# Optimization experiments

Measured on AMD Instinct MI355X. Metric: run time of the kernel, lower is better.

## Reference

```python
import jax, jax.numpy as jnp
import numpy as np

D = 2048
N_HEADS = 16
N_KV = 4
HEAD_DIM = D // N_HEADS  # 128
N_REP = N_HEADS // N_KV  # 4
B, S = 2, 2048


def setup_inputs() -> dict:
    key = jax.random.key(0)
    ks = jax.random.split(key, 5)
    scale = 0.02
    return {
        "x": jax.random.normal(ks[0], (B, S, D), dtype=jnp.float32),
        "wq": jax.random.normal(ks[1], (D, N_HEADS * HEAD_DIM), dtype=jnp.float32) * scale,
        "wk": jax.random.normal(ks[2], (D, N_KV * HEAD_DIM), dtype=jnp.float32) * scale,
        "wv": jax.random.normal(ks[3], (D, N_KV * HEAD_DIM), dtype=jnp.float32) * scale,
        "wo": jax.random.normal(ks[4], (N_HEADS * HEAD_DIM, D), dtype=jnp.float32) * scale,
    }


def reference(x, wq, wk, wv, wo):
    b, s, _ = x.shape
    # projections
    xq = (x @ wq).reshape(b, s, N_HEADS, HEAD_DIM)
    xk = (x @ wk).reshape(b, s, N_KV, HEAD_DIM)
    xv = (x @ wv).reshape(b, s, N_KV, HEAD_DIM)
    # GQA: group queries per kv head -> [b, n_kv, n_rep, s, d]
    xq = xq.transpose(0, 2, 1, 3).reshape(b, N_KV, N_REP, s, HEAD_DIM)
    xk = xk.transpose(0, 2, 1, 3)  # [b, n_kv, s, d]
    xv = xv.transpose(0, 2, 1, 3)
    scale = 1.0 / jnp.sqrt(jnp.asarray(HEAD_DIM, dtype=x.dtype))
    scores = jnp.einsum('bkrqd,bkvd->bkrqv', xq, xk) * scale  # [b,n_kv,n_rep,s,s]
    causal = jnp.triu(jnp.ones((s, s), dtype=bool), k=1)
    scores = jnp.where(causal, jnp.asarray(-jnp.inf, dtype=scores.dtype), scores)
    probs = jax.nn.softmax(scores, axis=-1)
    out = jnp.einsum('bkrqv,bkvd->bkrqd', probs, xv)  # [b,n_kv,n_rep,s,d]
    out = out.reshape(b, N_HEADS, s, HEAD_DIM).transpose(0, 2, 1, 3).reshape(b, s, N_HEADS * HEAD_DIM)
    return out @ wo
```

## Files before the change

### kernel.cpp

```cpp
#include <hip/hip_runtime.h>

typedef unsigned short u16;
using bf16x8 = __attribute__((ext_vector_type(8))) short;
using f32x4  = __attribute__((ext_vector_type(4))) float;

#define ATTN_NEG (-3.0e38f)

__device__ __forceinline__ u16 f2bf_rne(float f) {
  unsigned int u = __float_as_uint(f);
  u += 0x7fffu + ((u >> 16) & 1u);
  return (u16)(u >> 16);
}

__device__ __forceinline__ void load_lds16(const u16* g, u16* l) {
  using gp = const __attribute__((address_space(1))) unsigned int*;
  using lp = __attribute__((address_space(3))) unsigned int*;
  __builtin_amdgcn_global_load_lds((gp)g, (lp)l, 16, 0, 0);
}

__device__ __forceinline__ void transpose_body(const float* __restrict__ in,
                                               u16* __restrict__ out, int K, int N,
                                               int bx, int by, int tid) {
  __shared__ float tile[32][33];
  int tx = tid & 31, ty = tid >> 5;
  int x0 = bx * 32, y0 = by * 32;
  #pragma unroll
  for (int i = 0; i < 32; i += 8)
    tile[ty + i][tx] = in[(size_t)(y0 + ty + i) * N + x0 + tx];
  __syncthreads();
  #pragma unroll
  for (int i = 0; i < 32; i += 8)
    out[(size_t)(x0 + ty + i) * K + y0 + tx] = f2bf_rne(tile[tx][ty + i]);
}

__global__ __launch_bounds__(256) void prep_kernel(const float* __restrict__ x,
                                                   const float* __restrict__ wq,
                                                   const float* __restrict__ wk,
                                                   const float* __restrict__ wv,
                                                   const float* __restrict__ wo,
                                                   u16* xb, u16* wqt, u16* wkt, u16* wvt,
                                                   u16* wot) {
  int bid = blockIdx.x, tid = threadIdx.x;
  if (bid < 8192) {
    int i = bid * 1024 + tid * 4;
    float4 v = *(const float4*)(x + i);
    u16* p = xb + i;
    p[0] = f2bf_rne(v.x); p[1] = f2bf_rne(v.y); p[2] = f2bf_rne(v.z); p[3] = f2bf_rne(v.w);
  } else if (bid < 12288) {
    int t = bid - 8192;
    transpose_body(wq, wqt, 2048, 2048, t & 63, t >> 6, tid);
  } else if (bid < 13312) {
    int t = bid - 12288;
    transpose_body(wk, wkt, 2048, 512, t & 15, t >> 4, tid);
  } else if (bid < 14336) {
    int t = bid - 13312;
    transpose_body(wv, wvt, 2048, 512, t & 15, t >> 4, tid);
  } else {
    int t = bid - 14336;
    transpose_body(wo, wot, 2048, 2048, t & 63, t >> 6, tid);
  }
}

template <int MODE>
__device__ __forceinline__ void gemm_tile(const u16* __restrict__ A, const u16* __restrict__ Bt,
                                          void* __restrict__ Cv, int M, int N, int K,
                                          int bx, int by, char* smem) {
  u16* As = (u16*)smem;
  u16* Bs = (u16*)(smem + 8192);
  const int tid  = threadIdx.x;
  const int wave = tid >> 6, lane = tid & 63;
  const int quad = lane >> 4, l16 = lane & 15;
  const int m0 = by * 128, n0 = bx * 128;
  const int wm = (wave >> 1) * 64, wn = (wave & 1) * 64;
  f32x4 acc[4][4] = {};

  const int srow = (wave << 4) + (lane >> 2);
  const int scol = (lane & 3) << 3;
  const u16* ga0 = A  + (size_t)(m0 + srow) * K + scol;
  const u16* gb0 = Bt + (size_t)(n0 + srow) * K + scol;
  u16* la = As + wave * 512;
  u16* lb = Bs + wave * 512;

  for (int k0 = 0; k0 < K; k0 += 32) {
    __syncthreads();
    load_lds16(ga0 + k0, la);
    load_lds16(ga0 + (size_t)64 * K + k0, la + 2048);
    load_lds16(gb0 + k0, lb);
    load_lds16(gb0 + (size_t)64 * K + k0, lb + 2048);
    __syncthreads();
    bf16x8 af[4], bfr[4];
    #pragma unroll
    for (int i = 0; i < 4; ++i) {
      af[i]  = *(const bf16x8*)(As + (wm + i * 16 + l16) * 32 + quad * 8);
      bfr[i] = *(const bf16x8*)(Bs + (wn + i * 16 + l16) * 32 + quad * 8);
    }
    #pragma unroll
    for (int mi = 0; mi < 4; ++mi)
      #pragma unroll
      for (int ni = 0; ni < 4; ++ni)
        acc[mi][ni] = __builtin_amdgcn_mfma_f32_16x16x32_bf16(af[mi], bfr[ni], acc[mi][ni], 0, 0, 0);
  }

  if constexpr (MODE == 0 || MODE == 3) {
    const float sc = (MODE == 3) ? 0.12751742f : 1.0f;
    u16* Cb = (u16*)Cv;
    #pragma unroll
    for (int mi = 0; mi < 4; ++mi)
      #pragma unroll
      for (int ni = 0; ni < 4; ++ni) {
        int row = m0 + wm + mi * 16 + quad * 4;
        int col = n0 + wn + ni * 16 + l16;
        #pragma unroll
        for (int r = 0; r < 4; ++r)
          Cb[(size_t)(row + r) * N + col] = f2bf_rne(acc[mi][ni][r] * sc);
      }
  } else if constexpr (MODE == 1) {
    u16* Cb = (u16*)Cv;
    #pragma unroll
    for (int mi = 0; mi < 4; ++mi)
      #pragma unroll
      for (int ni = 0; ni < 4; ++ni) {
        int col = n0 + wn + ni * 16 + l16;
        #pragma unroll
        for (int r = 0; r < 4; ++r) {
          int row = m0 + wm + mi * 16 + quad * 4 + r;
          int bb = row >> 11, s = row & 2047;
          Cb[((size_t)(bb * 512 + col)) * 2048 + s] = f2bf_rne(acc[mi][ni][r]);
        }
      }
  } else {
    float* Cf = (float*)Cv;
    #pragma unroll
    for (int mi = 0; mi < 4; ++mi)
      #pragma unroll
      for (int ni = 0; ni < 4; ++ni) {
        int row = m0 + wm + mi * 16 + quad * 4;
        int col = n0 + wn + ni * 16 + l16;
        #pragma unroll
        for (int r = 0; r < 4; ++r)
          Cf[(size_t)(row + r) * N + col] = acc[mi][ni][r];
      }
  }
}

__global__ __launch_bounds__(256) void qkv_gemm(const u16* xb, const u16* wqt, const u16* wkt,
                                                const u16* wvt, u16* Qb, u16* Kb, u16* Vt) {
  extern __shared__ char smem[];
  int bx = blockIdx.x, by = blockIdx.y;
  if (bx < 16)
    gemm_tile<3>(xb, wqt, Qb, 4096, 2048, 2048, bx, by, smem);
  else if (bx < 20)
    gemm_tile<0>(xb, wkt, Kb, 4096, 512, 2048, bx - 16, by, smem);
  else
    gemm_tile<1>(xb, wvt, Vt, 4096, 512, 2048, bx - 20, by, smem);
}

template <int MODE>
__global__ __launch_bounds__(256) void gemm_kernel(const u16* A, const u16* Bt, void* C,
                                                   int M, int N, int K) {
  extern __shared__ char smem[];
  gemm_tile<MODE>(A, Bt, C, M, N, K, blockIdx.x, blockIdx.y, smem);
}


__device__ __forceinline__ void stage_kv(const u16* __restrict__ Kg, const u16* __restrict__ Vg,
                                         int kt0, u16* __restrict__ kbuf, u16* __restrict__ vbuf,
                                         int wave, int quad, int l16) {
  if (wave == 0) {
    #pragma unroll
    for (int ks = 0; ks < 4; ++ks)
      #pragma unroll
      for (int h = 0; h < 2; ++h)
        load_lds16(Kg + (size_t)(kt0 + h * 16 + l16) * 512 + ks * 32 + quad * 8,
                   kbuf + (ks * 2 + h) * 512);
  } else {
    #pragma unroll
    for (int f = 0; f < 8; ++f)
      load_lds16(Vg + (size_t)(16 * f + l16) * 2048 + kt0 + quad * 8, vbuf + f * 512);
  }
}

template <bool MASKED>
__device__ __forceinline__ void attn_compute(const u16* __restrict__ kbuf,
                                             const u16* __restrict__ vbuf,
                                             u16* __restrict__ pw, int kt0, int q0w,
                                             int quad, int l16, const bf16x8 (&qf)[4],
                                             f32x4 (&o)[8], float (&l_part)[4]) {
  const bool have1 = !MASKED || ((q0w & 16) != 0);
  const int slot = (quad * 16 + l16) * 8;
  f32x4 sa0 = {}, sa1 = {};
  #pragma unroll
  for (int ks = 0; ks < 4; ++ks) {
    bf16x8 kf0 = *(const bf16x8*)(kbuf + (ks * 2) * 512 + slot);
    sa0 = __builtin_amdgcn_mfma_f32_16x16x32_bf16(qf[ks], kf0, sa0, 0, 0, 0);
  }
  if (have1) {
    #pragma unroll
    for (int ks = 0; ks < 4; ++ks) {
      bf16x8 kf1 = *(const bf16x8*)(kbuf + (ks * 2 + 1) * 512 + slot);
      sa1 = __builtin_amdgcn_mfma_f32_16x16x32_bf16(qf[ks], kf1, sa1, 0, 0, 0);
    }
  }

  float p0[4], p1[4];
  #pragma unroll
  for (int r = 0; r < 4; ++r) {
    float s0, s1;
    if (MASKED) {
      int qpos = q0w + quad * 4 + r;
      s0 = (kt0 + l16 <= qpos) ? sa0[r] : ATTN_NEG;
      s1 = (have1 && (kt0 + 16 + l16 <= qpos)) ? sa1[r] : ATTN_NEG;
    } else {
      s0 = sa0[r];
      s1 = sa1[r];
    }
    p0[r] = __builtin_amdgcn_exp2f(s0);
    p1[r] = __builtin_amdgcn_exp2f(s1);
    l_part[r] += p0[r] + p1[r];
  }
  #pragma unroll
  for (int r = 0; r < 4; ++r) {
    pw[(quad * 4 + r) * 40 + l16]      = f2bf_rne(p0[r]);
    pw[(quad * 4 + r) * 40 + 16 + l16] = f2bf_rne(p1[r]);
  }
  __builtin_amdgcn_wave_barrier();
  bf16x8 pf = *(const bf16x8*)(pw + l16 * 40 + quad * 8);
  #pragma unroll
  for (int f = 0; f < 8; ++f) {
    bf16x8 vf = *(const bf16x8*)(vbuf + f * 512 + slot);
    o[f] = __builtin_amdgcn_mfma_f32_16x16x32_bf16(pf, vf, o[f], 0, 0, 0);
  }
}

__global__ __launch_bounds__(128, 2) void attn_kernel(const u16* __restrict__ Qb,
                                                      const u16* __restrict__ Kb,
                                                      const u16* __restrict__ Vt,
                                                      u16* __restrict__ Ob) {
  constexpr int S = 2048;
  const int b = blockIdx.z, h = blockIdx.y, g = h >> 2, tp = blockIdx.x;
  const int tid = threadIdx.x;
  const int wave = tid >> 6, lane = tid & 63, quad = lane >> 4, l16 = lane & 15;
  __shared__ alignas(16) u16 Kt[2][4096];
  __shared__ alignas(16) u16 Vl[2][4096];
  __shared__ alignas(16) u16 Pl[2][640];

  const u16* Kg = Kb + (size_t)b * S * 512 + g * 128;
  const u16* Vg = Vt + (size_t)(b * 512 + g * 128) * 2048;
  u16* pw = &Pl[wave][0];

  #pragma unroll
  for (int half = 0; half < 2; ++half) {
    const int tile = (half == 0) ? tp : 63 - tp;
    const int q0w = tile * 32 + wave * 16;
    const int nsteps = tile + 1;

    bf16x8 qf[4];
    const u16* qrow = Qb + (size_t)(b * S + q0w + l16) * 2048 + h * 128 + quad * 8;
    #pragma unroll
    for (int ks = 0; ks < 4; ++ks) qf[ks] = *(const bf16x8*)(qrow + ks * 32);

    f32x4 o[8] = {};
    float l_part[4] = {0.f, 0.f, 0.f, 0.f};

    __syncthreads();
    stage_kv(Kg, Vg, 0, Kt[0], Vl[0], wave, quad, l16);

    for (int s = 0; s < nsteps; ++s) {
      __syncthreads();
      if (s + 1 < nsteps)
        stage_kv(Kg, Vg, (s + 1) * 32, Kt[(s + 1) & 1], Vl[(s + 1) & 1], wave, quad, l16);
      if (s < nsteps - 1)
        attn_compute<false>(Kt[s & 1], Vl[s & 1], pw, s * 32, q0w, quad, l16, qf, o, l_part);
      else
        attn_compute<true>(Kt[s & 1], Vl[s & 1], pw, s * 32, q0w, quad, l16, qf, o, l_part);
    }

    #pragma unroll
    for (int d = 1; d < 16; d <<= 1) {
      #pragma unroll
      for (int r = 0; r < 4; ++r) l_part[r] += __shfl_xor(l_part[r], d);
    }
    float il[4];
    #pragma unroll
    for (int r = 0; r < 4; ++r) il[r] = 1.f / l_part[r];
    u16* orow = Ob + (size_t)(b * S + q0w + quad * 4) * 2048 + h * 128 + l16;
    #pragma unroll
    for (int f = 0; f < 8; ++f)
      #pragma unroll
      for (int r = 0; r < 4; ++r)
        orow[(size_t)r * 2048 + f * 16] = f2bf_rne(o[f][r] * il[r]);
  }
}

extern "C" void kernel_launch(void* const* d_in, const int* in_sizes, int n_in,
                              void* d_out, int out_size, void* d_ws, size_t ws_size,
                              hipStream_t stream) {
  const float* x  = (const float*)d_in[0];
  const float* wq = (const float*)d_in[1];
  const float* wk = (const float*)d_in[2];
  const float* wv = (const float*)d_in[3];
  const float* wo = (const float*)d_in[4];
  float* out = (float*)d_out;
  char* ws = (char*)d_ws;

  u16* xb  = (u16*)(ws);
  u16* wqt = (u16*)(ws + 16777216);
  u16* wkt = (u16*)(ws + 25165824);
  u16* wvt = (u16*)(ws + 27262976);
  u16* wot = (u16*)(ws + 29360128);
  u16* Qb  = (u16*)(ws + 37748736);
  u16* Kb  = (u16*)(ws + 54525952);
  u16* Vt  = (u16*)(ws + 58720256);
  u16* Ab  = (u16*)(ws + 62914560);

  prep_kernel<<<18432, 256, 0, stream>>>(x, wq, wk, wv, wo, xb, wqt, wkt, wvt, wot);
  qkv_gemm<<<dim3(24, 32), 256, 16384, stream>>>(xb, wqt, wkt, wvt, Qb, Kb, Vt);
  attn_kernel<<<dim3(32, 16, 2), 128, 0, stream>>>(Qb, Kb, Vt, Ab);
  gemm_kernel<2><<<dim3(16, 32), 256, 16384, stream>>>(Ab, wot, out, 4096, 2048, 2048);
}
```

Measured before the change: 348.0 us.

## Enlarge attention query tile to 128 rows with 4 waves sharing K/V stages

The attention kernel now uses 256-thread blocks covering 128 query rows. Each wave handles two 16-row query subtiles against the same K fragments in registers, so each staged K/V tile is reused across four times as many queries. All four waves now share the K/V staging loads. Causal skipping is done per wave using a diagonal step index, and tile pairing (tp, 15-tp) keeps the load balanced. The trade-offs are fewer blocks (256 instead of 1024), higher register pressure at occupancy 1, and waves that sit idle past their diagonal step but still hit the barriers.

After: 341.1 us. 1.02x faster.

```diff
diff --git a/kernel.cpp b/kernel.cpp
--- a/kernel.cpp
+++ b/kernel.cpp
@@ -166,73 +166,78 @@
 __device__ __forceinline__ void stage_kv(const u16* __restrict__ Kg, const u16* __restrict__ Vg,
                                          int kt0, u16* __restrict__ kbuf, u16* __restrict__ vbuf,
                                          int wave, int quad, int l16) {
-  if (wave == 0) {
-    #pragma unroll
-    for (int ks = 0; ks < 4; ++ks)
-      #pragma unroll
-      for (int h = 0; h < 2; ++h)
-        load_lds16(Kg + (size_t)(kt0 + h * 16 + l16) * 512 + ks * 32 + quad * 8,
-                   kbuf + (ks * 2 + h) * 512);
-  } else {
-    #pragma unroll
-    for (int f = 0; f < 8; ++f)
-      load_lds16(Vg + (size_t)(16 * f + l16) * 2048 + kt0 + quad * 8, vbuf + f * 512);
+  #pragma unroll
+  for (int h = 0; h < 2; ++h)
+    load_lds16(Kg + (size_t)(kt0 + h * 16 + l16) * 512 + wave * 32 + quad * 8,
+               kbuf + (wave * 2 + h) * 512);
+  #pragma unroll
+  for (int i = 0; i < 2; ++i) {
+    int f = wave * 2 + i;
+    load_lds16(Vg + (size_t)(16 * f + l16) * 2048 + kt0 + quad * 8, vbuf + f * 512);
   }
 }
 
 template <bool MASKED>
 __device__ __forceinline__ void attn_compute(const u16* __restrict__ kbuf,
                                              const u16* __restrict__ vbuf,
-                                             u16* __restrict__ pw, int kt0, int q0w,
-                                             int quad, int l16, const bf16x8 (&qf)[4],
-                                             f32x4 (&o)[8], float (&l_part)[4]) {
-  const bool have1 = !MASKED || ((q0w & 16) != 0);
+                                             u16* __restrict__ pw0, u16* __restrict__ pw1,
+                                             int kt0, int q0w, int quad, int l16,
+                                             const bf16x8 (&qf)[2][4], f32x4 (&o)[2][8],
+                                             float (&l_part)[2][4]) {
   const int slot = (quad * 16 + l16) * 8;
-  f32x4 sa0 = {}, sa1 = {};
-  #pragma unroll
-  for (int ks = 0; ks < 4; ++ks) {
-    bf16x8 kf0 = *(const bf16x8*)(kbuf + (ks * 2) * 512 + slot);
-    sa0 = __builtin_amdgcn_mfma_f32_16x16x32_bf16(qf[ks], kf0, sa0, 0, 0, 0);
-  }
-  if (have1) {
-    #pragma unroll
-    for (int ks = 0; ks < 4; ++ks) {
-      bf16x8 kf1 = *(const bf16x8*)(kbuf + (ks * 2 + 1) * 512 + slot);
-      sa1 = __builtin_amdgcn_mfma_f32_16x16x32_bf16(qf[ks], kf1, sa1, 0, 0, 0);
-    }
-  }
-
-  float p0[4], p1[4];
-  #pragma unroll
-  for (int r = 0; r < 4; ++r) {
-    float s0, s1;
-    if (MASKED) {
-      int qpos = q0w + quad * 4 + r;
-      s0 = (kt0 + l16 <= qpos) ? sa0[r] : ATTN_NEG;
-      s1 = (have1 && (kt0 + 16 + l16 <= qpos)) ? sa1[r] : ATTN_NEG;
-    } else {
-      s0 = sa0[r];
-      s1 = sa1[r];
-    }
-    p0[r] = __builtin_amdgcn_exp2f(s0);
-    p1[r] = __builtin_amdgcn_exp2f(s1);
-    l_part[r] += p0[r] + p1[r];
-  }
-  #pragma unroll
-  for (int r = 0; r < 4; ++r) {
-    pw[(quad * 4 + r) * 40 + l16]      = f2bf_rne(p0[r]);
-    pw[(quad * 4 + r) * 40 + 16 + l16] = f2bf_rne(p1[r]);
+  bf16x8 kf[8];
+  #pragma unroll
+  for (int kk = 0; kk < 8; ++kk) kf[kk] = *(const bf16x8*)(kbuf + kk * 512 + slot);
+
+  f32x4 sa[2][2] = {};
+  #pragma unroll
+  for (int j = 0; j < 2; ++j)
+    #pragma unroll
+    for (int h = 0; h < 2; ++h)
+      #pragma unroll
+      for (int ks = 0; ks < 4; ++ks)
+        sa[j][h] = __builtin_amdgcn_mfma_f32_16x16x32_bf16(qf[j][ks], kf[ks * 2 + h],
+                                                           sa[j][h], 0, 0, 0);
+
+  u16* pws[2] = {pw0, pw1};
+  #pragma unroll
+  for (int j = 0; j < 2; ++j) {
+    float p0[4], p1[4];
+    #pragma unroll
+    for (int r = 0; r < 4; ++r) {
+      float s0, s1;
+      if (MASKED) {
+        int qpos = q0w + j * 16 + quad * 4 + r;
+        s0 = (kt0 + l16 <= qpos) ? sa[j][0][r] : ATTN_NEG;
+        s1 = (kt0 + 16 + l16 <= qpos) ? sa[j][1][r] : ATTN_NEG;
+      } else {
+        s0 = sa[j][0][r];
+        s1 = sa[j][1][r];
+      }
+      p0[r] = __builtin_amdgcn_exp2f(s0);
+      p1[r] = __builtin_amdgcn_exp2f(s1);
+      l_part[j][r] += p0[r] + p1[r];
+    }
+    #pragma unroll
+    for (int r = 0; r < 4; ++r) {
+      pws[j][(quad * 4 + r) * 40 + l16]      = f2bf_rne(p0[r]);
+      pws[j][(quad * 4 + r) * 40 + 16 + l16] = f2bf_rne(p1[r]);
+    }
   }
   __builtin_amdgcn_wave_barrier();
-  bf16x8 pf = *(const bf16x8*)(pw + l16 * 40 + quad * 8);
+  bf16x8 pf[2];
+  pf[0] = *(const bf16x8*)(pw0 + l16 * 40 + quad * 8);
+  pf[1] = *(const bf16x8*)(pw1 + l16 * 40 + quad * 8);
   #pragma unroll
   for (int f = 0; f < 8; ++f) {
     bf16x8 vf = *(const bf16x8*)(vbuf + f * 512 + slot);
-    o[f] = __builtin_amdgcn_mfma_f32_16x16x32_bf16(pf, vf, o[f], 0, 0, 0);
-  }
-}
-
-__global__ __launch_bounds__(128, 2) void attn_kernel(const u16* __restrict__ Qb,
+    #pragma unroll
+    for (int j = 0; j < 2; ++j)
+      o[j][f] = __builtin_amdgcn_mfma_f32_16x16x32_bf16(pf[j], vf, o[j][f], 0, 0, 0);
+  }
+}
+
+__global__ __launch_bounds__(256, 1) void attn_kernel(const u16* __restrict__ Qb,
                                                       const u16* __restrict__ Kb,
                                                       const u16* __restrict__ Vt,
                                                       u16* __restrict__ Ob) {
@@ -242,25 +247,29 @@
   const int wave = tid >> 6, lane = tid & 63, quad = lane >> 4, l16 = lane & 15;
   __shared__ alignas(16) u16 Kt[2][4096];
   __shared__ alignas(16) u16 Vl[2][4096];
-  __shared__ alignas(16) u16 Pl[2][640];
+  __shared__ alignas(16) u16 Pl[4][2][640];
 
   const u16* Kg = Kb + (size_t)b * S * 512 + g * 128;
   const u16* Vg = Vt + (size_t)(b * 512 + g * 128) * 2048;
-  u16* pw = &Pl[wave][0];
 
   #pragma unroll
   for (int half = 0; half < 2; ++half) {
-    const int tile = (half == 0) ? tp : 63 - tp;
-    const int q0w = tile * 32 + wave * 16;
-    const int nsteps = tile + 1;
-
-    bf16x8 qf[4];
-    const u16* qrow = Qb + (size_t)(b * S + q0w + l16) * 2048 + h * 128 + quad * 8;
-    #pragma unroll
-    for (int ks = 0; ks < 4; ++ks) qf[ks] = *(const bf16x8*)(qrow + ks * 32);
-
-    f32x4 o[8] = {};
-    float l_part[4] = {0.f, 0.f, 0.f, 0.f};
+    const int tile = (half == 0) ? tp : 15 - tp;
+    const int wrow = (half == 0) ? wave : 3 - wave;
+    const int q0w = tile * 128 + wrow * 32;
+    const int nsteps = 4 * tile + 4;
+    const int s_diag = 4 * tile + wrow;
+
+    bf16x8 qf[2][4];
+    #pragma unroll
+    for (int j = 0; j < 2; ++j) {
+      const u16* qrow = Qb + (size_t)(b * S + q0w + j * 16 + l16) * 2048 + h * 128 + quad * 8;
+      #pragma unroll
+      for (int ks = 0; ks < 4; ++ks) qf[j][ks] = *(const bf16x8*)(qrow + ks * 32);
+    }
+
+    f32x4 o[2][8] = {};
+    float l_part[2][4] = {};
 
     __syncthreads();
     stage_kv(Kg, Vg, 0, Kt[0], Vl[0], wave, quad, l16);
@@ -269,26 +278,34 @@
       __syncthreads();
       if (s + 1 < nsteps)
         stage_kv(Kg, Vg, (s + 1) * 32, Kt[(s + 1) & 1], Vl[(s + 1) & 1], wave, quad, l16);
-      if (s < nsteps - 1)
-        attn_compute<false>(Kt[s & 1], Vl[s & 1], pw, s * 32, q0w, quad, l16, qf, o, l_part);
-      else
-        attn_compute<true>(Kt[s & 1], Vl[s & 1], pw, s * 32, q0w, quad, l16, qf, o, l_part);
-    }
-
-    #pragma unroll
-    for (int d = 1; d < 16; d <<= 1) {
-      #pragma unroll
-      for (int r = 0; r < 4; ++r) l_part[r] += __shfl_xor(l_part[r], d);
-    }
-    float il[4];
-    #pragma unroll
-    for (int r = 0; r < 4; ++r) il[r] = 1.f / l_part[r];
-    u16* orow = Ob + (size_t)(b * S + q0w + quad * 4) * 2048 + h * 128 + l16;
-    #pragma unroll
-    for (int f = 0; f < 8; ++f)
-      #pragma unroll
-      for (int r = 0; r < 4; ++r)
-        orow[(size_t)r * 2048 + f * 16] = f2bf_rne(o[f][r] * il[r]);
+      if (s < s_diag)
+        attn_compute<false>(Kt[s & 1], Vl[s & 1], &Pl[wave][0][0], &Pl[wave][1][0], s * 32,
+                            q0w, quad, l16, qf, o, l_part);
+      else if (s == s_diag)
+        attn_compute<true>(Kt[s & 1], Vl[s & 1], &Pl[wave][0][0], &Pl[wave][1][0], s * 32,
+                           q0w, quad, l16, qf, o, l_part);
+    }
+
+    #pragma unroll
+    for (int j = 0; j < 2; ++j) {
+      float lp[4];
+      #pragma unroll
+      for (int r = 0; r < 4; ++r) lp[r] = l_part[j][r];
+      #pragma unroll
+      for (int d = 1; d < 16; d <<= 1) {
+        #pragma unroll
+        for (int r = 0; r < 4; ++r) lp[r] += __shfl_xor(lp[r], d);
+      }
+      float il[4];
+      #pragma unroll
+      for (int r = 0; r < 4; ++r) il[r] = 1.f / lp[r];
+      u16* orow = Ob + (size_t)(b * S + q0w + j * 16 + quad * 4) * 2048 + h * 128 + l16;
+      #pragma unroll
+      for (int f = 0; f < 8; ++f)
+        #pragma unroll
+        for (int r = 0; r < 4; ++r)
+          orow[(size_t)r * 2048 + f * 16] = f2bf_rne(o[j][f][r] * il[r]);
+    }
   }
 }
 
@@ -315,6 +332,6 @@
 
   prep_kernel<<<18432, 256, 0, stream>>>(x, wq, wk, wv, wo, xb, wqt, wkt, wvt, wot);
   qkv_gemm<<<dim3(24, 32), 256, 16384, stream>>>(xb, wqt, wkt, wvt, Qb, Kb, Vt);
-  attn_kernel<<<dim3(32, 16, 2), 128, 0, stream>>>(Qb, Kb, Vt, Ab);
+  attn_kernel<<<dim3(8, 16, 2), 256, 0, stream>>>(Qb, Kb, Vt, Ab);
   gemm_kernel<2><<<dim3(16, 32), 256, 16384, stream>>>(Ab, wot, out, 4096, 2048, 2048);
 }
```

## Compute transposed scores to keep P in registers, enlarge attention tiles to 64 rows

Applied to the files above, without the earlier changes.

Attention now computes S^T (K as A operand), so each lane holds probabilities already laid out as the B operand of 16x16x16 MFMAs. This removes the per-wave LDS round trip for P. To match that layout, the V tensor written by the QKV GEMM uses a permuted sequence order within each 32-block. Blocks grow to 4 waves covering 64 query rows and share K/V staging, with per-wave diagonal skipping. Risks include the smaller-K MFMA instruction having lower throughput, the extra row-sum reduction through LDS, and idle steps for the upper waves.

After: 311.8 us. 1.12x faster.

```diff
diff --git a/kernel.cpp b/kernel.cpp
--- a/kernel.cpp
+++ b/kernel.cpp
@@ -2,9 +2,26 @@
 
 typedef unsigned short u16;
 using bf16x8 = __attribute__((ext_vector_type(8))) short;
+using bf16x4 = __attribute__((ext_vector_type(4))) short;
 using f32x4  = __attribute__((ext_vector_type(4))) float;
 
 #define ATTN_NEG (-3.0e38f)
+
+#if __has_builtin(__builtin_amdgcn_mfma_f32_16x16x16_bf16)
+__device__ __forceinline__ f32x4 mfma16(bf16x4 a, bf16x4 b, f32x4 c) {
+  return __builtin_amdgcn_mfma_f32_16x16x16_bf16(a, b, c, 0, 0, 0);
+}
+#elif __has_builtin(__builtin_amdgcn_mfma_f32_16x16x16bf16_1k)
+__device__ __forceinline__ f32x4 mfma16(bf16x4 a, bf16x4 b, f32x4 c) {
+  return __builtin_amdgcn_mfma_f32_16x16x16bf16_1k(a, b, c, 0, 0, 0);
+}
+#else
+__device__ __forceinline__ f32x4 mfma16(bf16x4 a, bf16x4 b, f32x4 c) {
+  asm volatile("v_mfma_f32_16x16x16_bf16 %0, %1, %2, %3"
+               : "=v"(c) : "v"(a), "v"(b), "v"(c));
+  return c;
+}
+#endif
 
 __device__ __forceinline__ u16 f2bf_rne(float f) {
   unsigned int u = __float_as_uint(f);
@@ -125,7 +142,9 @@
         for (int r = 0; r < 4; ++r) {
           int row = m0 + wm + mi * 16 + quad * 4 + r;
           int bb = row >> 11, s = row & 2047;
-          Cb[((size_t)(bb * 512 + col)) * 2048 + s] = f2bf_rne(acc[mi][ni][r]);
+          int c = s & 31;
+          int cp = ((c & 15) >> 2) * 8 + ((c >> 4) & 1) * 4 + (c & 3);
+          Cb[((size_t)(bb * 512 + col)) * 2048 + (s & ~31) + cp] = f2bf_rne(acc[mi][ni][r]);
         }
       }
   } else {
@@ -166,73 +185,62 @@
 __device__ __forceinline__ void stage_kv(const u16* __restrict__ Kg, const u16* __restrict__ Vg,
                                          int kt0, u16* __restrict__ kbuf, u16* __restrict__ vbuf,
                                          int wave, int quad, int l16) {
-  if (wave == 0) {
-    #pragma unroll
-    for (int ks = 0; ks < 4; ++ks)
-      #pragma unroll
-      for (int h = 0; h < 2; ++h)
-        load_lds16(Kg + (size_t)(kt0 + h * 16 + l16) * 512 + ks * 32 + quad * 8,
-                   kbuf + (ks * 2 + h) * 512);
-  } else {
-    #pragma unroll
-    for (int f = 0; f < 8; ++f)
-      load_lds16(Vg + (size_t)(16 * f + l16) * 2048 + kt0 + quad * 8, vbuf + f * 512);
+  #pragma unroll
+  for (int h = 0; h < 2; ++h)
+    load_lds16(Kg + (size_t)(kt0 + h * 16 + l16) * 512 + wave * 32 + quad * 8,
+               kbuf + (wave * 2 + h) * 512);
+  #pragma unroll
+  for (int i = 0; i < 2; ++i) {
+    int f = wave * 2 + i;
+    load_lds16(Vg + (size_t)(16 * f + l16) * 2048 + kt0 + quad * 8, vbuf + f * 512);
   }
 }
 
 template <bool MASKED>
 __device__ __forceinline__ void attn_compute(const u16* __restrict__ kbuf,
                                              const u16* __restrict__ vbuf,
-                                             u16* __restrict__ pw, int kt0, int q0w,
-                                             int quad, int l16, const bf16x8 (&qf)[4],
-                                             f32x4 (&o)[8], float (&l_part)[4]) {
-  const bool have1 = !MASKED || ((q0w & 16) != 0);
+                                             int kt0, int q0w, int quad, int l16,
+                                             const bf16x8 (&qf)[4], f32x4 (&o)[8],
+                                             float& l_lane) {
   const int slot = (quad * 16 + l16) * 8;
-  f32x4 sa0 = {}, sa1 = {};
-  #pragma unroll
-  for (int ks = 0; ks < 4; ++ks) {
-    bf16x8 kf0 = *(const bf16x8*)(kbuf + (ks * 2) * 512 + slot);
-    sa0 = __builtin_amdgcn_mfma_f32_16x16x32_bf16(qf[ks], kf0, sa0, 0, 0, 0);
-  }
-  if (have1) {
-    #pragma unroll
-    for (int ks = 0; ks < 4; ++ks) {
-      bf16x8 kf1 = *(const bf16x8*)(kbuf + (ks * 2 + 1) * 512 + slot);
-      sa1 = __builtin_amdgcn_mfma_f32_16x16x32_bf16(qf[ks], kf1, sa1, 0, 0, 0);
+  bf16x8 kf[8];
+  #pragma unroll
+  for (int kk = 0; kk < 8; ++kk) kf[kk] = *(const bf16x8*)(kbuf + kk * 512 + slot);
+
+  f32x4 sa[2] = {};
+  #pragma unroll
+  for (int h = 0; h < 2; ++h)
+    #pragma unroll
+    for (int ks = 0; ks < 4; ++ks)
+      sa[h] = __builtin_amdgcn_mfma_f32_16x16x32_bf16(kf[ks * 2 + h], qf[ks], sa[h], 0, 0, 0);
+
+  bf16x4 pa[2];
+  #pragma unroll
+  for (int h = 0; h < 2; ++h) {
+    #pragma unroll
+    for (int r = 0; r < 4; ++r) {
+      float s = sa[h][r];
+      if (MASKED) {
+        int kpos = kt0 + 16 * h + quad * 4 + r;
+        s = (kpos <= q0w + l16) ? s : ATTN_NEG;
+      }
+      float p = __builtin_amdgcn_exp2f(s);
+      l_lane += p;
+      pa[h][r] = (short)f2bf_rne(p);
     }
   }
 
-  float p0[4], p1[4];
-  #pragma unroll
-  for (int r = 0; r < 4; ++r) {
-    float s0, s1;
-    if (MASKED) {
-      int qpos = q0w + quad * 4 + r;
-      s0 = (kt0 + l16 <= qpos) ? sa0[r] : ATTN_NEG;
-      s1 = (have1 && (kt0 + 16 + l16 <= qpos)) ? sa1[r] : ATTN_NEG;
-    } else {
-      s0 = sa0[r];
-      s1 = sa1[r];
-    }
-    p0[r] = __builtin_amdgcn_exp2f(s0);
-    p1[r] = __builtin_amdgcn_exp2f(s1);
-    l_part[r] += p0[r] + p1[r];
-  }
-  #pragma unroll
-  for (int r = 0; r < 4; ++r) {
-    pw[(quad * 4 + r) * 40 + l16]      = f2bf_rne(p0[r]);
-    pw[(quad * 4 + r) * 40 + 16 + l16] = f2bf_rne(p1[r]);
-  }
-  __builtin_amdgcn_wave_barrier();
-  bf16x8 pf = *(const bf16x8*)(pw + l16 * 40 + quad * 8);
   #pragma unroll
   for (int f = 0; f < 8; ++f) {
-    bf16x8 vf = *(const bf16x8*)(vbuf + f * 512 + slot);
-    o[f] = __builtin_amdgcn_mfma_f32_16x16x32_bf16(pf, vf, o[f], 0, 0, 0);
-  }
-}
-
-__global__ __launch_bounds__(128, 2) void attn_kernel(const u16* __restrict__ Qb,
+    bf16x8 v8 = *(const bf16x8*)(vbuf + f * 512 + slot);
+    bf16x4 vlo = {v8[0], v8[1], v8[2], v8[3]};
+    bf16x4 vhi = {v8[4], v8[5], v8[6], v8[7]};
+    o[f] = mfma16(pa[0], vlo, o[f]);
+    o[f] = mfma16(pa[1], vhi, o[f]);
+  }
+}
+
+__global__ __launch_bounds__(256, 2) void attn_kernel(const u16* __restrict__ Qb,
                                                       const u16* __restrict__ Kb,
                                                       const u16* __restrict__ Vt,
                                                       u16* __restrict__ Ob) {
@@ -242,17 +250,18 @@
   const int wave = tid >> 6, lane = tid & 63, quad = lane >> 4, l16 = lane & 15;
   __shared__ alignas(16) u16 Kt[2][4096];
   __shared__ alignas(16) u16 Vl[2][4096];
-  __shared__ alignas(16) u16 Pl[2][640];
+  __shared__ float lbuf[4][16];
 
   const u16* Kg = Kb + (size_t)b * S * 512 + g * 128;
   const u16* Vg = Vt + (size_t)(b * 512 + g * 128) * 2048;
-  u16* pw = &Pl[wave][0];
 
   #pragma unroll
   for (int half = 0; half < 2; ++half) {
-    const int tile = (half == 0) ? tp : 63 - tp;
-    const int q0w = tile * 32 + wave * 16;
-    const int nsteps = tile + 1;
+    const int tile = (half == 0) ? tp : 31 - tp;
+    const int wrow = (half == 0) ? wave : 3 - wave;
+    const int q0w = tile * 64 + wrow * 16;
+    const int nsteps = 2 * tile + 2;
+    const int s_diag = 2 * tile + (wrow >> 1);
 
     bf16x8 qf[4];
     const u16* qrow = Qb + (size_t)(b * S + q0w + l16) * 2048 + h * 128 + quad * 8;
@@ -260,7 +269,7 @@
     for (int ks = 0; ks < 4; ++ks) qf[ks] = *(const bf16x8*)(qrow + ks * 32);
 
     f32x4 o[8] = {};
-    float l_part[4] = {0.f, 0.f, 0.f, 0.f};
+    float l_lane = 0.f;
 
     __syncthreads();
     stage_kv(Kg, Vg, 0, Kt[0], Vl[0], wave, quad, l16);
@@ -269,20 +278,20 @@
       __syncthreads();
       if (s + 1 < nsteps)
         stage_kv(Kg, Vg, (s + 1) * 32, Kt[(s + 1) & 1], Vl[(s + 1) & 1], wave, quad, l16);
-      if (s < nsteps - 1)
-        attn_compute<false>(Kt[s & 1], Vl[s & 1], pw, s * 32, q0w, quad, l16, qf, o, l_part);
-      else
-        attn_compute<true>(Kt[s & 1], Vl[s & 1], pw, s * 32, q0w, quad, l16, qf, o, l_part);
+      if (s < s_diag)
+        attn_compute<false>(Kt[s & 1], Vl[s & 1], s * 32, q0w, quad, l16, qf, o, l_lane);
+      else if (s == s_diag)
+        attn_compute<true>(Kt[s & 1], Vl[s & 1], s * 32, q0w, quad, l16, qf, o, l_lane);
     }
 
-    #pragma unroll
-    for (int d = 1; d < 16; d <<= 1) {
-      #pragma unroll
-      for (int r = 0; r < 4; ++r) l_part[r] += __shfl_xor(l_part[r], d);
-    }
+    float lt = l_lane + __shfl_xor(l_lane, 16);
+    lt += __shfl_xor(lt, 32);
+    if (quad == 0) lbuf[wave][l16] = lt;
+    __builtin_amdgcn_wave_barrier();
     float il[4];
     #pragma unroll
-    for (int r = 0; r < 4; ++r) il[r] = 1.f / l_part[r];
+    for (int r = 0; r < 4; ++r) il[r] = 1.f / lbuf[wave][quad * 4 + r];
+
     u16* orow = Ob + (size_t)(b * S + q0w + quad * 4) * 2048 + h * 128 + l16;
     #pragma unroll
     for (int f = 0; f < 8; ++f)
@@ -315,6 +324,6 @@
 
   prep_kernel<<<18432, 256, 0, stream>>>(x, wq, wk, wv, wo, xb, wqt, wkt, wvt, wot);
   qkv_gemm<<<dim3(24, 32), 256, 16384, stream>>>(xb, wqt, wkt, wvt, Qb, Kb, Vt);
-  attn_kernel<<<dim3(32, 16, 2), 128, 0, stream>>>(Qb, Kb, Vt, Ab);
+  attn_kernel<<<dim3(16, 16, 2), 256, 0, stream>>>(Qb, Kb, Vt, Ab);
   gemm_kernel<2><<<dim3(16, 32), 256, 16384, stream>>>(Ab, wot, out, 4096, 2048, 2048);
 }
```
